# Kernel tuning notes

Hardware: AMD Instinct MI355X
Metric: run time of the kernel (lower is better)

Reference implementation:

```python
import jax, jax.numpy as jnp
import numpy as np

EPS = 1e-5

def layernorm(x, g, b):
    mu = jnp.mean(x, axis=-1, keepdims=True)
    var = jnp.var(x, axis=-1, keepdims=True)
    return (x - mu) * jax.lax.rsqrt(var + EPS) * g + b

def setup_inputs() -> dict:
    key = jax.random.key(0)
    ks = jax.random.split(key, 12)
    B, T, C, H = 8, 2048, 64, 4
    d = C // H
    s = 0.02
    return {
        "x": jax.random.normal(ks[0], (B, T, C), jnp.float32),
        "Wq": jax.random.normal(ks[1], (H, C, d), jnp.float32) * s,
        "Wk": jax.random.normal(ks[2], (H, C, d), jnp.float32) * s,
        "Wv": jax.random.normal(ks[3], (H, C, d), jnp.float32) * s,
        "Wo": jax.random.normal(ks[4], (C, C), jnp.float32) * s,
        "bo": jnp.zeros((C,), jnp.float32),
        "W1": jax.random.normal(ks[5], (C, 4 * C), jnp.float32) * s,
        "bias1": jnp.zeros((4 * C,), jnp.float32),
        "W2": jax.random.normal(ks[6], (4 * C, C), jnp.float32) * s,
        "bias2": jnp.zeros((C,), jnp.float32),
        "gamma1": jnp.ones((C,), jnp.float32),
        "beta1": jnp.zeros((C,), jnp.float32),
        "gamma2": jnp.ones((C,), jnp.float32),
        "beta2": jnp.zeros((C,), jnp.float32),
    }

def reference(x, Wq, Wk, Wv, Wo, bo, W1, bias1, W2, bias2, gamma1, beta1, gamma2, beta2):
    B, T, C = x.shape
    H, _, d = Wq.shape
    # pre-LN attention
    h = layernorm(x, gamma1, beta1)
    q = jnp.einsum('btc,hcd->bhtd', h, Wq)
    k = jnp.einsum('btc,hcd->bhtd', h, Wk)
    v = jnp.einsum('btc,hcd->bhtd', h, Wv)
    scores = jnp.einsum('bhtd,bhsd->bhts', q, k) / jnp.sqrt(jnp.float32(d))
    causal = jnp.tril(jnp.ones((T, T), bool))
    scores = jnp.where(causal, scores, -jnp.inf)
    attn = jax.nn.softmax(scores, axis=-1)  # dropout = identity (eval)
    out = jnp.einsum('bhts,bhsd->bhtd', attn, v)
    out = out.transpose(0, 2, 1, 3).reshape(B, T, C)  # concat heads
    x = x + out @ Wo + bo
    # MLP
    h2 = layernorm(x, gamma2, beta2)
    x = x + jax.nn.relu(h2 @ W1 + bias1) @ W2 + bias2
    return x
```

## Files before the change

### kernel.cpp

```cpp
#include <hip/hip_runtime.h>

constexpr int Bn = 8, Tn = 2048;
constexpr int VS = 2080;

typedef __bf16 bf16x8 __attribute__((ext_vector_type(8)));
typedef float  f32x16 __attribute__((ext_vector_type(16)));
typedef short  short8 __attribute__((ext_vector_type(8)));
typedef unsigned short ushort_t;

__device__ __forceinline__ unsigned short f2bf(float f) {
    __bf16 h = (__bf16)f;
    return __builtin_bit_cast(unsigned short, h);
}

__device__ __forceinline__ float fast_exp2(float x) {
    float r;
    asm("v_exp_f32 %0, %1" : "=v"(r) : "v"(x));
    return r;
}

__device__ __forceinline__ unsigned cvt_pk_bf16(float lo, float hi_) {
    unsigned r;
    asm("v_cvt_pk_bf16_f32 %0, %1, %2" : "=v"(r) : "v"(lo), "v"(hi_));
    return r;
}

__device__ __forceinline__ bf16x8 xch_frag(
    float a0, float a1, float a2, float a3,
    float a4, float a5, float a6, float a7, int hi)
{
    const float s0 = hi ? a0 : a4, s1 = hi ? a1 : a5;
    const float s2 = hi ? a2 : a6, s3 = hi ? a3 : a7;
    const float r0 = __shfl_xor(s0, 32), r1 = __shfl_xor(s1, 32);
    const float r2 = __shfl_xor(s2, 32), r3 = __shfl_xor(s3, 32);
    bf16x8 f;
    f[0] = (__bf16)(hi ? r0 : a0); f[1] = (__bf16)(hi ? r1 : a1);
    f[2] = (__bf16)(hi ? r2 : a2); f[3] = (__bf16)(hi ? r3 : a3);
    f[4] = (__bf16)(hi ? a4 : r0); f[5] = (__bf16)(hi ? a5 : r1);
    f[6] = (__bf16)(hi ? a6 : r2); f[7] = (__bf16)(hi ? a7 : r3);
    return f;
}

__global__ __launch_bounds__(256) void k_prep(
    const float* __restrict__ Wo, const float* __restrict__ W1, const float* __restrict__ W2,
    const float* __restrict__ Wq, const float* __restrict__ Wk, const float* __restrict__ Wv,
    ushort_t* __restrict__ WoT, ushort_t* __restrict__ W1T, ushort_t* __restrict__ W2T,
    ushort_t* __restrict__ WqT, ushort_t* __restrict__ WkT, ushort_t* __restrict__ WvT)
{
    const int i = blockIdx.x * 256 + threadIdx.x;
    if (i < 4096) {
        const int n = i >> 6, k = i & 63;
        WoT[i] = f2bf(Wo[k * 64 + n]);
    } else if (i < 20480) {
        const int i2 = i - 4096, n = i2 >> 6, k = i2 & 63;
        W1T[i2] = f2bf(W1[k * 256 + n]);
    } else if (i < 36864) {
        const int i2 = i - 20480, n = i2 >> 8, k = i2 & 255;
        W2T[i2] = f2bf(W2[k * 64 + n]);
    } else if (i < 49152) {
        const int j = i - 36864;
        const int a = j >> 12, jj = j & 4095;
        const int n = jj >> 6, c = jj & 63;
        const int src = (n >> 4) * 1024 + c * 16 + (n & 15);
        const float v = (a == 0) ? Wq[src] : (a == 1) ? Wk[src] : Wv[src];
        ushort_t* dst = (a == 0) ? WqT : (a == 1) ? WkT : WvT;
        dst[jj] = f2bf(v);
    }
}

__global__ __launch_bounds__(256) void k_ln_qkv(
    const float* __restrict__ x,
    const ushort_t* __restrict__ WqT, const ushort_t* __restrict__ WkT,
    const ushort_t* __restrict__ WvT,
    const float* __restrict__ g1, const float* __restrict__ b1,
    ushort_t* __restrict__ Qb, ushort_t* __restrict__ Kb, ushort_t* __restrict__ VT)
{
    __shared__ ushort_t wl0[64 * 64], wl1[64 * 64], wl2[64 * 64];
    const int tid = threadIdx.x;
    #pragma unroll
    for (int it = 0; it < 2; ++it) {
        const int i = it * 256 + tid;
        const int r = i >> 3, c = i & 7;
        const int dst = r * 64 + ((c ^ (r & 7)) * 8);
        *(short8*)&wl0[dst] = *(const short8*)&WqT[i * 8];
        *(short8*)&wl1[dst] = *(const short8*)&WkT[i * 8];
        *(short8*)&wl2[dst] = *(const short8*)&WvT[i * 8];
    }
    __syncthreads();

    const int wave = tid >> 6, lane = tid & 63;
    const int tile = wave >> 1, u = wave & 1;
    const int hi = lane >> 5, m31 = lane & 31;
    const int tok = blockIdx.x * 64 + tile * 32 + m31;
    const int b = tok >> 11, t2 = tok & 2047;

    float xc[4][8];
    #pragma unroll
    for (int ks = 0; ks < 4; ++ks) {
        const float4 u0 = *(const float4*)(x + (size_t)tok * 64 + 16 * ks + 8 * hi);
        const float4 u1 = *(const float4*)(x + (size_t)tok * 64 + 16 * ks + 8 * hi + 4);
        xc[ks][0] = u0.x; xc[ks][1] = u0.y; xc[ks][2] = u0.z; xc[ks][3] = u0.w;
        xc[ks][4] = u1.x; xc[ks][5] = u1.y; xc[ks][6] = u1.z; xc[ks][7] = u1.w;
    }
    float s = 0.f, sq = 0.f;
    #pragma unroll
    for (int ks = 0; ks < 4; ++ks)
        #pragma unroll
        for (int e = 0; e < 8; ++e) { s += xc[ks][e]; sq += xc[ks][e] * xc[ks][e]; }
    s  += __shfl_xor(s,  32);
    sq += __shfl_xor(sq, 32);
    const float mu  = s * (1.f / 64.f);
    const float var = sq * (1.f / 64.f) - mu * mu;
    const float rs  = rsqrtf(var + 1e-5f);

    bf16x8 hf[4];
    #pragma unroll
    for (int ks = 0; ks < 4; ++ks) {
        const float4 gq0 = *(const float4*)(g1 + 16 * ks + 8 * hi);
        const float4 gq1 = *(const float4*)(g1 + 16 * ks + 8 * hi + 4);
        const float4 bq0 = *(const float4*)(b1 + 16 * ks + 8 * hi);
        const float4 bq1 = *(const float4*)(b1 + 16 * ks + 8 * hi + 4);
        hf[ks][0] = (__bf16)((xc[ks][0] - mu) * rs * gq0.x + bq0.x);
        hf[ks][1] = (__bf16)((xc[ks][1] - mu) * rs * gq0.y + bq0.y);
        hf[ks][2] = (__bf16)((xc[ks][2] - mu) * rs * gq0.z + bq0.z);
        hf[ks][3] = (__bf16)((xc[ks][3] - mu) * rs * gq0.w + bq0.w);
        hf[ks][4] = (__bf16)((xc[ks][4] - mu) * rs * gq1.x + bq1.x);
        hf[ks][5] = (__bf16)((xc[ks][5] - mu) * rs * gq1.y + bq1.y);
        hf[ks][6] = (__bf16)((xc[ks][6] - mu) * rs * gq1.z + bq1.z);
        hf[ks][7] = (__bf16)((xc[ks][7] - mu) * rs * gq1.w + bq1.w);
    }

    f32x16 q = {}, k = {}, v = {};
    const int rw = m31 + 32 * u;
    #pragma unroll
    for (int ks = 0; ks < 4; ++ks) {
        const int ch = 2 * ks + hi;
        const int wo = rw * 64 + ((ch ^ (rw & 7)) * 8);
        const bf16x8 aq = *(const bf16x8*)&wl0[wo];
        const bf16x8 ak = *(const bf16x8*)&wl1[wo];
        const bf16x8 av = *(const bf16x8*)&wl2[wo];
        q = __builtin_amdgcn_mfma_f32_32x32x16_bf16(aq, hf[ks], q, 0, 0, 0);
        k = __builtin_amdgcn_mfma_f32_32x32x16_bf16(ak, hf[ks], k, 0, 0, 0);
        v = __builtin_amdgcn_mfma_f32_32x32x16_bf16(av, hf[ks], v, 0, 0, 0);
    }

    const float SC = 0.360673760222f;
    #pragma unroll
    for (int qd = 0; qd < 4; ++qd) {
        const int hd0 = 8 * qd + 4 * hi + 32 * u;
        const int hh = hd0 >> 4, d0 = hd0 & 15;
        const int r0 = 4 * qd;
        const size_t off = ((size_t)(b * 4 + hh) * Tn + t2) * 16 + d0;
        uint2 uq, uk;
        uq.x = cvt_pk_bf16(q[r0] * SC,   q[r0+1] * SC);
        uq.y = cvt_pk_bf16(q[r0+2] * SC, q[r0+3] * SC);
        uk.x = cvt_pk_bf16(k[r0],  k[r0+1]);
        uk.y = cvt_pk_bf16(k[r0+2], k[r0+3]);
        *(uint2*)(Qb + off) = uq;
        *(uint2*)(Kb + off) = uk;
    }
    #pragma unroll
    for (int r = 0; r < 16; ++r) {
        const int hd = (r & 3) + 8 * (r >> 2) + 4 * hi + 32 * u;
        const int hh = hd >> 4, d = hd & 15;
        VT[((size_t)(b * 4 + hh) * 32 + d) * VS + t2] = f2bf(v[r]);
    }
    if (u == 0) {
        #pragma unroll
        for (int hh = 0; hh < 4; ++hh)
            VT[((size_t)(b * 4 + hh) * 32 + 16) * VS + t2] = 0x3F80;
    }
}

#define EXP_PACK_PV(ST, V0, V1)                                                 \
    {                                                                           \
        float p[16];                                                            \
        _Pragma("unroll")                                                       \
        for (int r = 0; r < 16; ++r) p[r] = fast_exp2((ST)[r]);                 \
        const unsigned w0 = cvt_pk_bf16(p[0],  p[1]),  w1 = cvt_pk_bf16(p[2],  p[3]); \
        const unsigned w2 = cvt_pk_bf16(p[4],  p[5]),  w3 = cvt_pk_bf16(p[6],  p[7]); \
        const unsigned w4 = cvt_pk_bf16(p[8],  p[9]),  w5 = cvt_pk_bf16(p[10], p[11]); \
        const unsigned w6 = cvt_pk_bf16(p[12], p[13]), w7 = cvt_pk_bf16(p[14], p[15]); \
        const unsigned r0 = __shfl_xor(hi ? w0 : w2, 32);                       \
        const unsigned r1 = __shfl_xor(hi ? w1 : w3, 32);                       \
        const unsigned r2 = __shfl_xor(hi ? w4 : w6, 32);                       \
        const unsigned r3 = __shfl_xor(hi ? w5 : w7, 32);                       \
        union { unsigned u[4]; bf16x8 v; } pa0, pa1;                            \
        pa0.u[0] = hi ? r0 : w0;  pa0.u[1] = hi ? r1 : w1;                      \
        pa0.u[2] = hi ? w2 : r0;  pa0.u[3] = hi ? w3 : r1;                      \
        pa1.u[0] = hi ? r2 : w4;  pa1.u[1] = hi ? r3 : w5;                      \
        pa1.u[2] = hi ? w6 : r2;  pa1.u[3] = hi ? w7 : r3;                      \
        oacc = __builtin_amdgcn_mfma_f32_32x32x16_bf16(V0, pa0.v, oacc, 0, 0, 0); \
        oacc = __builtin_amdgcn_mfma_f32_32x32x16_bf16(V1, pa1.v, oacc, 0, 0, 0); \
    }

#define TILE(KF, V0, V1)                                                        \
    {                                                                           \
        __builtin_amdgcn_s_setprio(1);                                          \
        f32x16 st = __builtin_amdgcn_mfma_f32_32x32x16_bf16(KF, qf, CINIT, 0, 0, 0); \
        EXP_PACK_PV(st, V0, V1);                                                \
        __builtin_amdgcn_s_setprio(0);                                          \
    }

#define LOADKV(KF, V0, V1, KT)                                                  \
    {                                                                           \
        KF = *(const bf16x8*)(kaddr + (size_t)(KT) * 512);                      \
        V0 = *(const bf16x8*)(vaddr + (KT) * 32);                               \
        V1 = *(const bf16x8*)(vaddr + (KT) * 32 + 16);                          \
    }

__global__ __launch_bounds__(256) void k_attn(
    const ushort_t* __restrict__ Qb, const ushort_t* __restrict__ Kb,
    const ushort_t* __restrict__ VT, ushort_t* __restrict__ AOb)
{
    const int wave = threadIdx.x >> 6, lane = threadIdx.x & 63;
    const int xcd = blockIdx.x & 7;
    const int q_  = blockIdx.x >> 3;
    const int bh  = xcd * 4 + (q_ >> 5);
    const int qtA = q_ & 31;
    const int w = wave;
    const int hi = lane >> 5, qcol = lane & 31;
    const int b = bh >> 2, h = bh & 3;

    const int vrow_i = (lane & 31) > 16 ? 16 : (lane & 31);
    const ushort_t* Qbh = Qb + (size_t)bh * (Tn * 16);
    const ushort_t* kaddr = Kb + (size_t)bh * (Tn * 16) + (size_t)qcol * 16 + 8 * hi;
    const ushort_t* vaddr = VT + (size_t)bh * (32 * VS) + (size_t)vrow_i * VS + 8 * hi;

    __shared__ float red[4][2][64][12];

    f32x16 CINIT;
    #pragma unroll
    for (int r = 0; r < 16; ++r) CINIT[r] = -12.0f;

    for (int rep = 0; rep < 2; ++rep) {
        const int qt = rep ? (63 - qtA) : qtA;

        const bf16x8 qf = *(const bf16x8*)(Qbh + (size_t)(qt * 32 + qcol) * 16 + 8 * hi);

        f32x16 oacc = {};

        if ((qt & 3) == w) {
            const bf16x8 kfD = *(const bf16x8*)(kaddr + (size_t)qt * 512);
            const bf16x8 v0D = *(const bf16x8*)(vaddr + qt * 32);
            const bf16x8 v1D = *(const bf16x8*)(vaddr + qt * 32 + 16);
            __builtin_amdgcn_s_setprio(1);
            f32x16 st = __builtin_amdgcn_mfma_f32_32x32x16_bf16(kfD, qf, CINIT, 0, 0, 0);
            #pragma unroll
            for (int r = 0; r < 16; ++r) {
                const int kr = (r & 3) + 8 * (r >> 2) + 4 * hi;
                st[r] = (kr > qcol) ? -30000.f : st[r];
            }
            EXP_PACK_PV(st, v0D, v1D);
            __builtin_amdgcn_s_setprio(0);
        }

        if (qt - 1 >= w) {
            const int last = qt - 1 - ((qt - 1 - w) & 3);
            bf16x8 kfA, v0A, v1A, kfB, v0B, v1B, kfC, v0C, v1C;
            const int ktB0 = (w + 4 <= last) ? (w + 4) : last;
            const int ktC0 = (w + 8 <= last) ? (w + 8) : last;
            LOADKV(kfA, v0A, v1A, w);
            LOADKV(kfB, v0B, v1B, ktB0);
            LOADKV(kfC, v0C, v1C, ktC0);

            int kt = w;
            for (; kt + 8 <= last; kt += 12) {
                TILE(kfA, v0A, v1A);
                {
                    const int kn = (kt + 12 <= last) ? (kt + 12) : last;
                    LOADKV(kfA, v0A, v1A, kn);
                }
                TILE(kfB, v0B, v1B);
                {
                    const int kn = (kt + 16 <= last) ? (kt + 16) : last;
                    LOADKV(kfB, v0B, v1B, kn);
                }
                TILE(kfC, v0C, v1C);
                {
                    const int kn = (kt + 20 <= last) ? (kt + 20) : last;
                    LOADKV(kfC, v0C, v1C, kn);
                }
            }
            if (kt <= last)     TILE(kfA, v0A, v1A);
            if (kt + 4 <= last) TILE(kfB, v0B, v1B);
        }

        const float lo_ = __shfl_xor(oacc[8], 32);
        const float l = hi ? lo_ : oacc[8];

        float* sp = &red[wave][rep][lane][0];
        sp[0] = l;
        #pragma unroll
        for (int r = 0; r < 8; ++r) sp[1 + r] = oacc[r];
    }
    __syncthreads();

    if (wave < 2) {
        const int r_m = wave;
        const float* p0 = &red[0][r_m][lane][0];
        const float* p1 = &red[1][r_m][lane][0];
        const float* p2 = &red[2][r_m][lane][0];
        const float* p3 = &red[3][r_m][lane][0];
        const float lt = (p0[0] + p1[0]) + (p2[0] + p3[0]);
        const float inv = 1.f / lt;

        const int qt_out = r_m ? (63 - qtA) : qtA;
        const int qg2 = qt_out * 32 + qcol;

        float o[8];
        #pragma unroll
        for (int r = 0; r < 8; ++r)
            o[r] = ((p0[1 + r] + p1[1 + r]) + (p2[1 + r] + p3[1 + r])) * inv;

        ushort_t* dst = AOb + ((size_t)b * Tn + qg2) * 64 + h * 16;
        ushort4 u0, u1;
        u0.x = f2bf(o[0]); u0.y = f2bf(o[1]); u0.z = f2bf(o[2]); u0.w = f2bf(o[3]);
        u1.x = f2bf(o[4]); u1.y = f2bf(o[5]); u1.z = f2bf(o[6]); u1.w = f2bf(o[7]);
        *(ushort4*)(dst + 4 * hi)     = u0;
        *(ushort4*)(dst + 8 + 4 * hi) = u1;
    }
}

__global__ __launch_bounds__(256) void k_mlp(
    const float* __restrict__ x, const ushort_t* __restrict__ AOb,
    const ushort_t* __restrict__ WoTg, const float* __restrict__ bo,
    const float* __restrict__ g2, const float* __restrict__ b2v,
    const ushort_t* __restrict__ W1Tg, const float* __restrict__ bias1,
    const ushort_t* __restrict__ W2Tg, const float* __restrict__ bias2,
    float* __restrict__ out)
{
    __shared__ ushort_t wo_l[64 * 64];
    __shared__ ushort_t w1_l[256 * 64];
    __shared__ ushort_t w2_l[64 * 256];
    __shared__ float part[2][64][34];
    const int tid = threadIdx.x;
    #pragma unroll
    for (int it = 0; it < 2; ++it) {
        const int i = it * 256 + tid;
        const int r = i >> 3, c = i & 7;
        *(short8*)&wo_l[r * 64 + ((c ^ (r & 7)) * 8)] = *(const short8*)&WoTg[i * 8];
    }
    #pragma unroll
    for (int it = 0; it < 8; ++it) {
        const int i = it * 256 + tid;
        const int r = i >> 3, c = i & 7;
        *(short8*)&w1_l[r * 64 + ((c ^ (r & 7)) * 8)] = *(const short8*)&W1Tg[i * 8];
    }
    #pragma unroll
    for (int it = 0; it < 8; ++it) {
        const int i = it * 256 + tid;
        const int r = i >> 5, c = i & 31;
        *(short8*)&w2_l[r * 256 + ((c ^ (r & 7)) * 8)] = *(const short8*)&W2Tg[i * 8];
    }
    __syncthreads();

    const int wave = tid >> 6, lane = tid & 63;
    const int tile = wave >> 1, u = wave & 1;
    const int hi = lane >> 5, m31 = lane & 31;
    const size_t m = (size_t)(blockIdx.x * 2 + tile) * 32 + m31;

    f32x16 y0 = {}, y1 = {};
    {
        const ushort_t* ar = AOb + m * 64 + 8 * hi;
        const int r0 = m31, r1 = m31 + 32;
        #pragma unroll
        for (int ks = 0; ks < 4; ++ks) {
            const int ch = 2 * ks + hi;
            const bf16x8 bf = *(const bf16x8*)(ar + 16 * ks);
            const bf16x8 a0 = *(const bf16x8*)&wo_l[r0 * 64 + ((ch ^ (r0 & 7)) * 8)];
            const bf16x8 a1 = *(const bf16x8*)&wo_l[r1 * 64 + ((ch ^ (r1 & 7)) * 8)];
            y0 = __builtin_amdgcn_mfma_f32_32x32x16_bf16(a0, bf, y0, 0, 0, 0);
            y1 = __builtin_amdgcn_mfma_f32_32x32x16_bf16(a1, bf, y1, 0, 0, 0);
        }
    }

    #pragma unroll
    for (int q2 = 0; q2 < 4; ++q2) {
        {
            const int nb = 8 * q2 + 4 * hi;
            const float4 xq = *(const float4*)(x + m * 64 + nb);
            const float4 bq = *(const float4*)(bo + nb);
            y0[4*q2+0] += xq.x + bq.x; y0[4*q2+1] += xq.y + bq.y;
            y0[4*q2+2] += xq.z + bq.z; y0[4*q2+3] += xq.w + bq.w;
        }
        {
            const int nb = 32 + 8 * q2 + 4 * hi;
            const float4 xq = *(const float4*)(x + m * 64 + nb);
            const float4 bq = *(const float4*)(bo + nb);
            y1[4*q2+0] += xq.x + bq.x; y1[4*q2+1] += xq.y + bq.y;
            y1[4*q2+2] += xq.z + bq.z; y1[4*q2+3] += xq.w + bq.w;
        }
    }

    float s = 0.f, sq = 0.f;
    #pragma unroll
    for (int r = 0; r < 16; ++r) {
        s  += y0[r] + y1[r];
        sq += y0[r] * y0[r] + y1[r] * y1[r];
    }
    s  += __shfl_xor(s,  32);
    sq += __shfl_xor(sq, 32);
    const float mu  = s * (1.f / 64.f);
    const float var = sq * (1.f / 64.f) - mu * mu;
    const float rs  = rsqrtf(var + 1e-5f);

    float hreg[32];
    #pragma unroll
    for (int q2 = 0; q2 < 4; ++q2) {
        {
            const int nb = 8 * q2 + 4 * hi;
            const float4 gq = *(const float4*)(g2 + nb);
            const float4 bq = *(const float4*)(b2v + nb);
            hreg[4*q2+0] = (y0[4*q2+0] - mu) * rs * gq.x + bq.x;
            hreg[4*q2+1] = (y0[4*q2+1] - mu) * rs * gq.y + bq.y;
            hreg[4*q2+2] = (y0[4*q2+2] - mu) * rs * gq.z + bq.z;
            hreg[4*q2+3] = (y0[4*q2+3] - mu) * rs * gq.w + bq.w;
        }
        {
            const int nb = 32 + 8 * q2 + 4 * hi;
            const float4 gq = *(const float4*)(g2 + nb);
            const float4 bq = *(const float4*)(b2v + nb);
            hreg[16+4*q2+0] = (y1[4*q2+0] - mu) * rs * gq.x + bq.x;
            hreg[16+4*q2+1] = (y1[4*q2+1] - mu) * rs * gq.y + bq.y;
            hreg[16+4*q2+2] = (y1[4*q2+2] - mu) * rs * gq.z + bq.z;
            hreg[16+4*q2+3] = (y1[4*q2+3] - mu) * rs * gq.w + bq.w;
        }
    }

    f32x16 o0 = {}, o1 = {};
    #pragma unroll
    for (int gi = 0; gi < 4; ++gi) {
        const int g = 4 * u + gi;
        f32x16 hacc = {};
        #pragma unroll
        for (int ks = 0; ks < 4; ++ks) {
            const int base = 16 * (ks >> 1) + 8 * (ks & 1);
            const bf16x8 bf = xch_frag(hreg[base+0], hreg[base+1], hreg[base+2], hreg[base+3],
                                       hreg[base+4], hreg[base+5], hreg[base+6], hreg[base+7], hi);
            const int rw = 32 * g + m31;
            const int ch = 2 * ks + hi;
            const bf16x8 a = *(const bf16x8*)&w1_l[rw * 64 + ((ch ^ (rw & 7)) * 8)];
            hacc = __builtin_amdgcn_mfma_f32_32x32x16_bf16(a, bf, hacc, 0, 0, 0);
        }
        float hv[16];
        #pragma unroll
        for (int q2 = 0; q2 < 4; ++q2) {
            const int nb = 32 * g + 8 * q2 + 4 * hi;
            const float4 bq = *(const float4*)(bias1 + nb);
            hv[4*q2+0] = fmaxf(hacc[4*q2+0] + bq.x, 0.f);
            hv[4*q2+1] = fmaxf(hacc[4*q2+1] + bq.y, 0.f);
            hv[4*q2+2] = fmaxf(hacc[4*q2+2] + bq.z, 0.f);
            hv[4*q2+3] = fmaxf(hacc[4*q2+3] + bq.w, 0.f);
        }
        #pragma unroll
        for (int w2 = 0; w2 < 2; ++w2) {
            const int base = 8 * w2;
            const bf16x8 bf = xch_frag(hv[base+0], hv[base+1], hv[base+2], hv[base+3],
                                       hv[base+4], hv[base+5], hv[base+6], hv[base+7], hi);
            const int ch = 4 * g + 2 * w2 + hi;
            const int r0 = m31, r1 = m31 + 32;
            const bf16x8 a0 = *(const bf16x8*)&w2_l[r0 * 256 + ((ch ^ (r0 & 7)) * 8)];
            const bf16x8 a1 = *(const bf16x8*)&w2_l[r1 * 256 + ((ch ^ (r1 & 7)) * 8)];
            o0 = __builtin_amdgcn_mfma_f32_32x32x16_bf16(a0, bf, o0, 0, 0, 0);
            o1 = __builtin_amdgcn_mfma_f32_32x32x16_bf16(a1, bf, o1, 0, 0, 0);
        }
    }

    if (u == 1) {
        #pragma unroll
        for (int j = 0; j < 8; ++j) {
            float2 a = make_float2(o0[2*j], o0[2*j+1]);
            float2 bb = make_float2(o1[2*j], o1[2*j+1]);
            *(float2*)&part[tile][lane][2*j]      = a;
            *(float2*)&part[tile][lane][16 + 2*j] = bb;
        }
    }
    __syncthreads();
    if (u == 0) {
        #pragma unroll
        for (int r = 0; r < 16; ++r) {
            o0[r] += part[tile][lane][r];
            o1[r] += part[tile][lane][16 + r];
        }
        #pragma unroll
        for (int q2 = 0; q2 < 4; ++q2) {
            {
                const int nb = 8 * q2 + 4 * hi;
                const float4 bq = *(const float4*)(bias2 + nb);
                float4 r;
                r.x = y0[4*q2+0] + o0[4*q2+0] + bq.x;
                r.y = y0[4*q2+1] + o0[4*q2+1] + bq.y;
                r.z = y0[4*q2+2] + o0[4*q2+2] + bq.z;
                r.w = y0[4*q2+3] + o0[4*q2+3] + bq.w;
                *(float4*)(out + m * 64 + nb) = r;
            }
            {
                const int nb = 32 + 8 * q2 + 4 * hi;
                const float4 bq = *(const float4*)(bias2 + nb);
                float4 r;
                r.x = y1[4*q2+0] + o1[4*q2+0] + bq.x;
                r.y = y1[4*q2+1] + o1[4*q2+1] + bq.y;
                r.z = y1[4*q2+2] + o1[4*q2+2] + bq.z;
                r.w = y1[4*q2+3] + o1[4*q2+3] + bq.w;
                *(float4*)(out + m * 64 + nb) = r;
            }
        }
    }
}

extern "C" void kernel_launch(void* const* d_in, const int* in_sizes, int n_in,
                              void* d_out, int out_size, void* d_ws, size_t ws_size,
                              hipStream_t stream)
{
    const float* x     = (const float*)d_in[0];
    const float* Wq    = (const float*)d_in[1];
    const float* Wk    = (const float*)d_in[2];
    const float* Wv    = (const float*)d_in[3];
    const float* Wo    = (const float*)d_in[4];
    const float* bo    = (const float*)d_in[5];
    const float* W1    = (const float*)d_in[6];
    const float* bias1 = (const float*)d_in[7];
    const float* W2    = (const float*)d_in[8];
    const float* bias2 = (const float*)d_in[9];
    const float* g1    = (const float*)d_in[10];
    const float* be1   = (const float*)d_in[11];
    const float* g2    = (const float*)d_in[12];
    const float* be2   = (const float*)d_in[13];

    const size_t nBF = (size_t)32 * Tn * 16;
    ushort_t* Qb  = (ushort_t*)d_ws;
    ushort_t* Kb  = Qb + nBF;
    ushort_t* VT  = Kb + nBF;
    ushort_t* AOb = VT + (size_t)32 * 32 * VS;
    ushort_t* WoT = AOb + nBF;
    ushort_t* W1T = WoT + 4096;
    ushort_t* W2T = W1T + 16384;
    ushort_t* WqT = W2T + 16384;
    ushort_t* WkT = WqT + 4096;
    ushort_t* WvT = WkT + 4096;

    k_prep<<<dim3(192), dim3(256), 0, stream>>>(Wo, W1, W2, Wq, Wk, Wv,
                                                WoT, W1T, W2T, WqT, WkT, WvT);
    k_ln_qkv<<<dim3((Bn * Tn) / 64), dim3(256), 0, stream>>>(
        x, WqT, WkT, WvT, g1, be1, Qb, Kb, VT);
    k_attn<<<dim3(32 * 32), dim3(256), 0, stream>>>(Qb, Kb, VT, AOb);
    k_mlp<<<dim3((Bn * Tn) / 64), dim3(256), 0, stream>>>(
        x, AOb, WoT, bo, g2, be2, W1T, bias1, W2T, bias2, (float*)d_out);
}
```

Baseline: 41.59 us.

## Share K/V tile loads across both paired query tiles in attention kernel

The two query tiles handled by each block (qtA and 63-qtA) were processed in sequence, each loading its own K/V tiles. Now both query fragments are kept live and every K/V tile below the first tile's diagonal is loaded once and used for both accumulators. After that the second tile continues alone up to its own diagonal. The s_setprio hints are removed and the prefetch depth drops from three buffers to two. This cuts global K/V loads for the overlapping range, but it raises register pressure and changes the latency-hiding depth.

```diff
diff --git a/kernel.cpp b/kernel.cpp
--- a/kernel.cpp
+++ b/kernel.cpp
@@ -172,34 +172,43 @@
     }
 }
 
-#define EXP_PACK_PV(ST, V0, V1)                                                 \
+#define EXP_PACK_PV(ST, OACC, V0, V1)                                           \
     {                                                                           \
         float p[16];                                                            \
         _Pragma("unroll")                                                       \
         for (int r = 0; r < 16; ++r) p[r] = fast_exp2((ST)[r]);                 \
-        const unsigned w0 = cvt_pk_bf16(p[0],  p[1]),  w1 = cvt_pk_bf16(p[2],  p[3]); \
-        const unsigned w2 = cvt_pk_bf16(p[4],  p[5]),  w3 = cvt_pk_bf16(p[6],  p[7]); \
-        const unsigned w4 = cvt_pk_bf16(p[8],  p[9]),  w5 = cvt_pk_bf16(p[10], p[11]); \
-        const unsigned w6 = cvt_pk_bf16(p[12], p[13]), w7 = cvt_pk_bf16(p[14], p[15]); \
-        const unsigned r0 = __shfl_xor(hi ? w0 : w2, 32);                       \
-        const unsigned r1 = __shfl_xor(hi ? w1 : w3, 32);                       \
-        const unsigned r2 = __shfl_xor(hi ? w4 : w6, 32);                       \
-        const unsigned r3 = __shfl_xor(hi ? w5 : w7, 32);                       \
+        const unsigned pw0 = cvt_pk_bf16(p[0],  p[1]),  pw1 = cvt_pk_bf16(p[2],  p[3]); \
+        const unsigned pw2 = cvt_pk_bf16(p[4],  p[5]),  pw3 = cvt_pk_bf16(p[6],  p[7]); \
+        const unsigned pw4 = cvt_pk_bf16(p[8],  p[9]),  pw5 = cvt_pk_bf16(p[10], p[11]); \
+        const unsigned pw6 = cvt_pk_bf16(p[12], p[13]), pw7 = cvt_pk_bf16(p[14], p[15]); \
+        const unsigned pr0 = __shfl_xor(hi ? pw0 : pw2, 32);                    \
+        const unsigned pr1 = __shfl_xor(hi ? pw1 : pw3, 32);                    \
+        const unsigned pr2 = __shfl_xor(hi ? pw4 : pw6, 32);                    \
+        const unsigned pr3 = __shfl_xor(hi ? pw5 : pw7, 32);                    \
         union { unsigned u[4]; bf16x8 v; } pa0, pa1;                            \
-        pa0.u[0] = hi ? r0 : w0;  pa0.u[1] = hi ? r1 : w1;                      \
-        pa0.u[2] = hi ? w2 : r0;  pa0.u[3] = hi ? w3 : r1;                      \
-        pa1.u[0] = hi ? r2 : w4;  pa1.u[1] = hi ? r3 : w5;                      \
-        pa1.u[2] = hi ? w6 : r2;  pa1.u[3] = hi ? w7 : r3;                      \
-        oacc = __builtin_amdgcn_mfma_f32_32x32x16_bf16(V0, pa0.v, oacc, 0, 0, 0); \
-        oacc = __builtin_amdgcn_mfma_f32_32x32x16_bf16(V1, pa1.v, oacc, 0, 0, 0); \
-    }
-
-#define TILE(KF, V0, V1)                                                        \
+        pa0.u[0] = hi ? pr0 : pw0;  pa0.u[1] = hi ? pr1 : pw1;                  \
+        pa0.u[2] = hi ? pw2 : pr0;  pa0.u[3] = hi ? pw3 : pr1;                  \
+        pa1.u[0] = hi ? pr2 : pw4;  pa1.u[1] = hi ? pr3 : pw5;                  \
+        pa1.u[2] = hi ? pw6 : pr2;  pa1.u[3] = hi ? pw7 : pr3;                  \
+        OACC = __builtin_amdgcn_mfma_f32_32x32x16_bf16(V0, pa0.v, OACC, 0, 0, 0); \
+        OACC = __builtin_amdgcn_mfma_f32_32x32x16_bf16(V1, pa1.v, OACC, 0, 0, 0); \
+    }
+
+#define TILE(QF, OACC, KF, V0, V1)                                              \
     {                                                                           \
-        __builtin_amdgcn_s_setprio(1);                                          \
-        f32x16 st = __builtin_amdgcn_mfma_f32_32x32x16_bf16(KF, qf, CINIT, 0, 0, 0); \
-        EXP_PACK_PV(st, V0, V1);                                                \
-        __builtin_amdgcn_s_setprio(0);                                          \
+        f32x16 st = __builtin_amdgcn_mfma_f32_32x32x16_bf16(KF, QF, CINIT, 0, 0, 0); \
+        EXP_PACK_PV(st, OACC, V0, V1);                                          \
+    }
+
+#define DIAG_TILE(QF, OACC, QCMP, KF, V0, V1)                                   \
+    {                                                                           \
+        f32x16 st = __builtin_amdgcn_mfma_f32_32x32x16_bf16(KF, QF, CINIT, 0, 0, 0); \
+        _Pragma("unroll")                                                       \
+        for (int r = 0; r < 16; ++r) {                                          \
+            const int kr = (r & 3) + 8 * (r >> 2) + 4 * hi;                     \
+            st[r] = (kr > (QCMP)) ? -30000.f : st[r];                           \
+        }                                                                       \
+        EXP_PACK_PV(st, OACC, V0, V1);                                          \
     }
 
 #define LOADKV(KF, V0, V1, KT)                                                  \
@@ -233,66 +242,96 @@
     #pragma unroll
     for (int r = 0; r < 16; ++r) CINIT[r] = -12.0f;
 
-    for (int rep = 0; rep < 2; ++rep) {
-        const int qt = rep ? (63 - qtA) : qtA;
-
-        const bf16x8 qf = *(const bf16x8*)(Qbh + (size_t)(qt * 32 + qcol) * 16 + 8 * hi);
-
-        f32x16 oacc = {};
-
-        if ((qt & 3) == w) {
-            const bf16x8 kfD = *(const bf16x8*)(kaddr + (size_t)qt * 512);
-            const bf16x8 v0D = *(const bf16x8*)(vaddr + qt * 32);
-            const bf16x8 v1D = *(const bf16x8*)(vaddr + qt * 32 + 16);
-            __builtin_amdgcn_s_setprio(1);
-            f32x16 st = __builtin_amdgcn_mfma_f32_32x32x16_bf16(kfD, qf, CINIT, 0, 0, 0);
-            #pragma unroll
-            for (int r = 0; r < 16; ++r) {
-                const int kr = (r & 3) + 8 * (r >> 2) + 4 * hi;
-                st[r] = (kr > qcol) ? -30000.f : st[r];
+    const int qt0 = qtA;
+    const int qt1 = 63 - qtA;
+
+    const bf16x8 qf0 = *(const bf16x8*)(Qbh + (size_t)(qt0 * 32 + qcol) * 16 + 8 * hi);
+    const bf16x8 qf1 = *(const bf16x8*)(Qbh + (size_t)(qt1 * 32 + qcol) * 16 + 8 * hi);
+
+    f32x16 oacc0 = {}, oacc1 = {};
+
+    if (qt0 - 1 >= w) {
+        const int last0 = qt0 - 1 - ((qt0 - 1 - w) & 3);
+        bf16x8 kfA, v0A, v1A, kfB, v0B, v1B;
+        const int ktB0 = (w + 4 <= last0) ? (w + 4) : last0;
+        LOADKV(kfA, v0A, v1A, w);
+        LOADKV(kfB, v0B, v1B, ktB0);
+
+        int kt = w;
+        for (; kt + 4 <= last0; kt += 8) {
+            TILE(qf0, oacc0, kfA, v0A, v1A);
+            TILE(qf1, oacc1, kfA, v0A, v1A);
+            {
+                const int kn = (kt + 8 <= last0) ? (kt + 8) : last0;
+                LOADKV(kfA, v0A, v1A, kn);
             }
-            EXP_PACK_PV(st, v0D, v1D);
-            __builtin_amdgcn_s_setprio(0);
-        }
-
-        if (qt - 1 >= w) {
-            const int last = qt - 1 - ((qt - 1 - w) & 3);
-            bf16x8 kfA, v0A, v1A, kfB, v0B, v1B, kfC, v0C, v1C;
-            const int ktB0 = (w + 4 <= last) ? (w + 4) : last;
-            const int ktC0 = (w + 8 <= last) ? (w + 8) : last;
-            LOADKV(kfA, v0A, v1A, w);
+            TILE(qf0, oacc0, kfB, v0B, v1B);
+            TILE(qf1, oacc1, kfB, v0B, v1B);
+            {
+                const int kn = (kt + 12 <= last0) ? (kt + 12) : last0;
+                LOADKV(kfB, v0B, v1B, kn);
+            }
+        }
+        if (kt <= last0) {
+            TILE(qf0, oacc0, kfA, v0A, v1A);
+            TILE(qf1, oacc1, kfA, v0A, v1A);
+        }
+    }
+
+    if ((qt0 & 3) == w) {
+        bf16x8 kfD, v0D, v1D;
+        LOADKV(kfD, v0D, v1D, qt0);
+        DIAG_TILE(qf0, oacc0, qcol, kfD, v0D, v1D);
+        TILE(qf1, oacc1, kfD, v0D, v1D);
+    }
+
+    {
+        const int first2 = w + (((qt0 - w + 4) >> 2) << 2);
+        const int last1  = qt1 - 1 - ((qt1 - 1 - w) & 3);
+        if (first2 <= last1) {
+            bf16x8 kfA, v0A, v1A, kfB, v0B, v1B;
+            const int ktB0 = (first2 + 4 <= last1) ? (first2 + 4) : last1;
+            LOADKV(kfA, v0A, v1A, first2);
             LOADKV(kfB, v0B, v1B, ktB0);
-            LOADKV(kfC, v0C, v1C, ktC0);
-
-            int kt = w;
-            for (; kt + 8 <= last; kt += 12) {
-                TILE(kfA, v0A, v1A);
+
+            int kt = first2;
+            for (; kt + 4 <= last1; kt += 8) {
+                TILE(qf1, oacc1, kfA, v0A, v1A);
                 {
-                    const int kn = (kt + 12 <= last) ? (kt + 12) : last;
+                    const int kn = (kt + 8 <= last1) ? (kt + 8) : last1;
                     LOADKV(kfA, v0A, v1A, kn);
                 }
-                TILE(kfB, v0B, v1B);
+                TILE(qf1, oacc1, kfB, v0B, v1B);
                 {
-                    const int kn = (kt + 16 <= last) ? (kt + 16) : last;
+                    const int kn = (kt + 12 <= last1) ? (kt + 12) : last1;
                     LOADKV(kfB, v0B, v1B, kn);
                 }
-                TILE(kfC, v0C, v1C);
-                {
-                    const int kn = (kt + 20 <= last) ? (kt + 20) : last;
-                    LOADKV(kfC, v0C, v1C, kn);
-                }
             }
-            if (kt <= last)     TILE(kfA, v0A, v1A);
-            if (kt + 4 <= last) TILE(kfB, v0B, v1B);
-        }
-
-        const float lo_ = __shfl_xor(oacc[8], 32);
-        const float l = hi ? lo_ : oacc[8];
-
-        float* sp = &red[wave][rep][lane][0];
-        sp[0] = l;
-        #pragma unroll
-        for (int r = 0; r < 8; ++r) sp[1 + r] = oacc[r];
+            if (kt <= last1) TILE(qf1, oacc1, kfA, v0A, v1A);
+        }
+    }
+
+    if ((qt1 & 3) == w) {
+        bf16x8 kfD, v0D, v1D;
+        LOADKV(kfD, v0D, v1D, qt1);
+        DIAG_TILE(qf1, oacc1, qcol, kfD, v0D, v1D);
+    }
+
+    {
+        const float lo0 = __shfl_xor(oacc0[8], 32);
+        const float l0 = hi ? lo0 : oacc0[8];
+        float* sp = &red[wave][0][lane][0];
+        sp[0] = l0;
+        #pragma unroll
+        for (int r = 0; r < 8; ++r) sp[1 + r] = oacc0[r];
+    }
+    {
+        const float lo1 = __shfl_xor(oacc1[8], 32);
+        const float l1 = hi ? lo1 : oacc1[8];
+        float* sp = &red[wave][1][lane][0];
+        sp[0] = l1;
+        #pragma unroll
+        for (int r = 0; r < 8; ++r) sp[1 + r] = oacc1[r];
     }
     __syncthreads();
 
@@ -305,7 +344,7 @@
         const float lt = (p0[0] + p1[0]) + (p2[0] + p3[0]);
         const float inv = 1.f / lt;
 
-        const int qt_out = r_m ? (63 - qtA) : qtA;
+        const int qt_out = r_m ? qt1 : qt0;
         const int qg2 = qt_out * 32 + qcol;
 
         float o[8];
```

New measurement: 41.20 us. Within noise of the previous version (-0.9%).
